# Optimization experiments

Hardware: AMD Instinct MI355X
Metric: run time of the kernel (lower is better)

The kernel has to match this reference:

```python
import jax, jax.numpy as jnp
import numpy as np

NEG_INF = -9.0e15  # matches torch's -9000000000000000.0 mask value
ALPHA = 0.2        # LeakyReLU negative slope from init_kwargs


def setup_inputs() -> dict:
    key = jax.random.key(0)
    k1, k2, k3, k4, k5 = jax.random.split(key, 5)
    B, N, D, A = 64, 128, 128, 1000
    hidden = jax.random.normal(k1, (B, N, D), dtype=jnp.float32)
    adj = jax.random.randint(k2, (B, N, N), 0, 5)  # edge types 0..4 (0 = masked)
    a = jax.random.normal(k3, (D, 4), dtype=jnp.float32) * 0.1  # stacked a_0..a_3
    A_attr_sess = jax.random.uniform(k4, (B, N, A), dtype=jnp.float32)
    attr_embedding = jax.random.normal(k5, (A, D), dtype=jnp.float32)
    return {"hidden": hidden, "adj": adj, "a": a,
            "A_attr_sess": A_attr_sess, "attr_embedding": attr_embedding}


def reference(hidden, adj, a, A_attr_sess, attr_embedding):
    # a_input[b,i,j,:] = leaky_relu(h[b,i,:] * h[b,j,:])  -> [B,N,N,D]
    a_input = jax.nn.leaky_relu(hidden[:, :, None, :] * hidden[:, None, :, :],
                                negative_slope=ALPHA)
    # four edge-type scores in one contraction: [B,N,N,4]
    e = jnp.einsum('bijd,dk->bijk', a_input, a)
    # masked selection by adjacency edge type (later writes override earlier)
    alpha = jnp.full(adj.shape, NEG_INF, dtype=e.dtype)
    alpha = jnp.where(adj == 1, e[..., 0], alpha)
    alpha = jnp.where(adj == 2, e[..., 1], alpha)
    alpha = jnp.where(adj == 3, e[..., 2], alpha)
    alpha = jnp.where(adj == 4, e[..., 3], alpha)
    attn = jax.nn.softmax(alpha, axis=-1)        # [B,N,N]
    output = jnp.einsum('bij,bjd->bid', attn, hidden)  # [B,N,D]
    attr_sess = jnp.einsum('bna,ad->bnd', A_attr_sess, attr_embedding)
    return output, attr_sess
```

## Files before the change

### kernel.cpp

```cpp
#include <hip/hip_runtime.h>

#define BB 64
#define NN 128
#define DD 128
#define AA 1000
#define KPAD 1024
#define NEG_INF (-9.0e15f)

typedef __attribute__((ext_vector_type(8))) short short8;
typedef __attribute__((ext_vector_type(4))) float floatx4;
typedef __attribute__((ext_vector_type(4))) unsigned int uintx4;
typedef __attribute__((ext_vector_type(2))) unsigned int uintx2;

__device__ __forceinline__ float bflo(unsigned int u) { return __uint_as_float(u << 16); }
__device__ __forceinline__ float bfhi(unsigned int u) { return __uint_as_float(u & 0xffff0000u); }
__device__ __forceinline__ unsigned int packbf(float f0, float f1) {
  return (__float_as_uint(f0) >> 16) | (__float_as_uint(f1) & 0xffff0000u);
}
__device__ __forceinline__ unsigned short bf_rne(float f) {
  unsigned int u = __float_as_uint(f);
  return (unsigned short)((u + 0x7fffu + ((u >> 16) & 1u)) >> 16);
}
__device__ __forceinline__ unsigned int packbf_rne(float f0, float f1) {
  return (unsigned int)bf_rne(f0) | ((unsigned int)bf_rne(f1) << 16);
}
__device__ __forceinline__ short8 u2s(uintx4 v) {
  union { uintx4 u; short8 s; } x; x.u = v; return x.s;
}

__global__ __launch_bounds__(256) void prep_kernel(
    const float* __restrict__ hidden, const float* __restrict__ emb,
    unsigned short* __restrict__ ET, unsigned short* __restrict__ HTg)
{
  __shared__ float hsf[NN * 129];
  const int t = threadIdx.x;
  const int bid = blockIdx.x;
  if (bid < BB) {
    const float* hb = hidden + (size_t)bid * NN * DD;
    #pragma unroll
    for (int u = 0; u < 16; ++u) {
      int e = u * 1024 + t * 4;
      float4 v = *reinterpret_cast<const float4*>(hb + e);
      int r = e >> 7, c = e & 127;
      float* d = &hsf[r * 129 + c];
      d[0] = v.x; d[1] = v.y; d[2] = v.z; d[3] = v.w;
    }
    __syncthreads();
    unsigned short* ht16 = HTg + (size_t)bid * NN * DD;
    #pragma unroll
    for (int u = 0; u < 8; ++u) {
      int e = u * 2048 + t * 8;
      int dI = e >> 7, il = e & 127;
      float x[8];
      #pragma unroll
      for (int j = 0; j < 8; ++j) x[j] = hsf[(il + j) * 129 + dI];
      uintx4 o;
      o.x = packbf_rne(x[0], x[1]); o.y = packbf_rne(x[2], x[3]);
      o.z = packbf_rne(x[4], x[5]); o.w = packbf_rne(x[6], x[7]);
      *reinterpret_cast<uintx4*>(ht16 + e) = o;
    }
  } else {
    const int k0 = (bid - BB) * 32;
    #pragma unroll
    for (int u = 0; u < 4; ++u) {
      int e = u * 1024 + t * 4;
      int r = e >> 7, c = e & 127;
      float4 z = {0.f, 0.f, 0.f, 0.f};
      float4 v = (k0 + r < AA)
          ? *reinterpret_cast<const float4*>(emb + (size_t)(k0 + r) * DD + c) : z;
      float* d = &hsf[r * 129 + c];
      d[0] = v.x; d[1] = v.y; d[2] = v.z; d[3] = v.w;
    }
    __syncthreads();
    int c = t >> 1, j0 = (t & 1) * 16;
    float x[16];
    #pragma unroll
    for (int j = 0; j < 16; ++j) x[j] = hsf[(j0 + j) * 129 + c];
    uintx4 o0, o1;
    o0.x = packbf_rne(x[0], x[1]);  o0.y = packbf_rne(x[2], x[3]);
    o0.z = packbf_rne(x[4], x[5]);  o0.w = packbf_rne(x[6], x[7]);
    o1.x = packbf_rne(x[8], x[9]);  o1.y = packbf_rne(x[10], x[11]);
    o1.z = packbf_rne(x[12], x[13]); o1.w = packbf_rne(x[14], x[15]);
    unsigned short* dst = ET + (size_t)c * KPAD + k0 + j0;
    *reinterpret_cast<uintx4*>(dst) = o0;
    *reinterpret_cast<uintx4*>(dst + 8) = o1;
  }
}

struct AttnSmem {
  __align__(16) unsigned short Hs[NN * 128];
  union {
    __align__(16) unsigned short As[4 * 16 * 256];
    struct {
      __align__(16) float Sa[16 * 129];
      __align__(16) unsigned short W[16 * 128];
    } sw;
  } u2;
  __align__(16) float saf[4 * 256];
};

#define BK 64
struct AttrSmem {
  __align__(16) unsigned short ETs[2][DD * BK];
  __align__(16) unsigned short As2[2][16 * BK];
};

union FusedSmem { AttnSmem a; AttrSmem g; };

__device__ __forceinline__ void attn_body(
    AttnSmem& s, const float* __restrict__ hidden,
    const int* __restrict__ adj, const float* __restrict__ amat,
    const unsigned short* __restrict__ HTg, float* __restrict__ out0,
    int wid)
{
  const int t = threadIdx.x;
  const int L = t & 63, w = t >> 6;
  const int lr = L & 15, lq = L >> 4;
  const int b = wid >> 3;
  const int i0 = (wid & 7) * 16;

  const int* adjb = adj + ((size_t)b * NN + i0) * NN;
  int adjv[8];
  #pragma unroll
  for (int nt = 0; nt < 2; ++nt)
    #pragma unroll
    for (int r = 0; r < 4; ++r)
      adjv[nt * 4 + r] = adjb[(lq * 4 + r) * NN + w * 32 + nt * 16 + lr];

  const float* hb = hidden + (size_t)b * NN * DD;
  #pragma unroll
  for (int u = 0; u < 8; ++u) {
    int id = u * 256 + t;
    int r = id >> 4, c = id & 15;
    const float* src = hb + r * 128 + c * 8;
    float4 v0 = *reinterpret_cast<const float4*>(src);
    float4 v1 = *reinterpret_cast<const float4*>(src + 4);
    uintx4 o;
    o.x = packbf_rne(v0.x, v0.y); o.y = packbf_rne(v0.z, v0.w);
    o.z = packbf_rne(v1.x, v1.y); o.w = packbf_rne(v1.z, v1.w);
    *reinterpret_cast<uintx4*>(&s.Hs[r * 128 + ((c ^ (r & 15)) << 3)]) = o;
  }
  {
    float v1 = amat[t], v2 = amat[t + 256];
    int dI = t >> 2, k = t & 3;
    s.saf[k * 256 + dI] = 0.6f * v1;
    s.saf[k * 256 + 128 + dI] = 0.4f * v1;
    s.saf[k * 256 + 64 + dI] = 0.6f * v2;
    s.saf[k * 256 + 192 + dI] = 0.4f * v2;
  }
  __syncthreads();

  #pragma unroll
  for (int u = 0; u < 8; ++u) {
    int id = u * 256 + t;
    int k = id >> 9, ii = (id >> 5) & 15, c = id & 31;
    int srow = i0 + ii;
    int dchunk = c & 15;
    uintx4 hv = *reinterpret_cast<const uintx4*>(
        &s.Hs[srow * 128 + ((dchunk ^ (srow & 15)) << 3)]);
    if (c & 16) {
      hv.x &= 0x7fff7fffu; hv.y &= 0x7fff7fffu;
      hv.z &= 0x7fff7fffu; hv.w &= 0x7fff7fffu;
    }
    const float* sf = &s.saf[k * 256 + c * 8];
    uintx4 o;
    o.x = packbf(bflo(hv.x) * sf[0], bfhi(hv.x) * sf[1]);
    o.y = packbf(bflo(hv.y) * sf[2], bfhi(hv.y) * sf[3]);
    o.z = packbf(bflo(hv.z) * sf[4], bfhi(hv.z) * sf[5]);
    o.w = packbf(bflo(hv.w) * sf[6], bfhi(hv.w) * sf[7]);
    *reinterpret_cast<uintx4*>(&s.u2.As[k * 4096 + ii * 256 + ((c ^ ii) << 3)]) = o;
  }
  __syncthreads();

  floatx4 acc[4][2];
  #pragma unroll
  for (int k = 0; k < 4; ++k)
    #pragma unroll
    for (int nt = 0; nt < 2; ++nt) acc[k][nt] = floatx4{0.f, 0.f, 0.f, 0.f};

  #pragma unroll
  for (int kt = 0; kt < 8; ++kt) {
    int ca = lq + 4 * kt;
    short8 afr[4];
    #pragma unroll
    for (int k = 0; k < 4; ++k)
      afr[k] = *reinterpret_cast<const short8*>(
          &s.u2.As[k * 4096 + lr * 256 + ((ca ^ lr) << 3)]);
    int cb = lq + 4 * (kt & 3);
    short8 bfr[2];
    #pragma unroll
    for (int nt = 0; nt < 2; ++nt) {
      int jrow = w * 32 + nt * 16 + lr;
      uintx4 hv = *reinterpret_cast<const uintx4*>(
          &s.Hs[jrow * 128 + ((cb ^ (jrow & 15)) << 3)]);
      if (kt >= 4) {
        hv.x &= 0x7fff7fffu; hv.y &= 0x7fff7fffu;
        hv.z &= 0x7fff7fffu; hv.w &= 0x7fff7fffu;
      }
      bfr[nt] = u2s(hv);
    }
    #pragma unroll
    for (int k = 0; k < 4; ++k)
      #pragma unroll
      for (int nt = 0; nt < 2; ++nt)
        acc[k][nt] = __builtin_amdgcn_mfma_f32_16x16x32_bf16(
            afr[k], bfr[nt], acc[k][nt], 0, 0, 0);
  }
  __syncthreads();

  short8 pvb[2][4];
  const unsigned short* ht = HTg + (size_t)b * NN * DD;
  #pragma unroll
  for (int nt = 0; nt < 2; ++nt)
    #pragma unroll
    for (int kt = 0; kt < 4; ++kt) {
      int dI = w * 32 + nt * 16 + lr;
      pvb[nt][kt] = *reinterpret_cast<const short8*>(ht + dI * 128 + kt * 32 + lq * 8);
    }

  #pragma unroll
  for (int nt = 0; nt < 2; ++nt)
    #pragma unroll
    for (int r = 0; r < 4; ++r) {
      int ii = lq * 4 + r;
      int j = w * 32 + nt * 16 + lr;
      int ad = adjv[nt * 4 + r];
      float al = NEG_INF;
      al = (ad == 1) ? acc[0][nt][r] : al;
      al = (ad == 2) ? acc[1][nt][r] : al;
      al = (ad == 3) ? acc[2][nt][r] : al;
      al = (ad == 4) ? acc[3][nt][r] : al;
      s.u2.sw.Sa[ii * 129 + j] = al;
    }
  __syncthreads();

  #pragma unroll
  for (int p = 0; p < 4; ++p) {
    int ii = w * 4 + p;
    float a1 = s.u2.sw.Sa[ii * 129 + L];
    float a2 = s.u2.sw.Sa[ii * 129 + 64 + L];
    float m = fmaxf(a1, a2);
    #pragma unroll
    for (int off = 32; off > 0; off >>= 1) m = fmaxf(m, __shfl_xor(m, off, 64));
    float e1 = __expf(fmaxf(a1 - m, -80.f));
    float e2 = __expf(fmaxf(a2 - m, -80.f));
    float ss = e1 + e2;
    #pragma unroll
    for (int off = 32; off > 0; off >>= 1) ss += __shfl_xor(ss, off, 64);
    float inv = 1.f / ss;
    int j2 = L + 64;
    s.u2.sw.W[ii * 128 + (((L >> 3) ^ ii) << 3) + (L & 7)] = bf_rne(e1 * inv);
    s.u2.sw.W[ii * 128 + (((j2 >> 3) ^ ii) << 3) + (j2 & 7)] = bf_rne(e2 * inv);
  }
  __syncthreads();

  floatx4 oacc[2];
  oacc[0] = floatx4{0.f, 0.f, 0.f, 0.f};
  oacc[1] = floatx4{0.f, 0.f, 0.f, 0.f};
  #pragma unroll
  for (int kt = 0; kt < 4; ++kt) {
    int c = lq + 4 * kt;
    short8 wf = *reinterpret_cast<const short8*>(
        &s.u2.sw.W[lr * 128 + ((c ^ lr) << 3)]);
    #pragma unroll
    for (int nt = 0; nt < 2; ++nt)
      oacc[nt] = __builtin_amdgcn_mfma_f32_16x16x32_bf16(
          wf, pvb[nt][kt], oacc[nt], 0, 0, 0);
  }
  float* ob = out0 + ((size_t)b * NN + i0) * DD;
  #pragma unroll
  for (int nt = 0; nt < 2; ++nt)
    #pragma unroll
    for (int r = 0; r < 4; ++r)
      ob[(lq * 4 + r) * DD + w * 32 + nt * 16 + lr] = oacc[nt][r];
}

__device__ __forceinline__ void attr_body(
    AttrSmem& s, const float* __restrict__ Aattr,
    const unsigned short* __restrict__ ET, float* __restrict__ out1,
    int wid)
{
  const int t = threadIdx.x;
  const int L = t & 63, w = t >> 6;
  const int lr = L & 15, lq = L >> 4;
  const int r0 = wid * 16;

  const int ar = t >> 4;
  const int ak = (t & 15) * 4;
  const int ec = t >> 1, ej0 = (t & 1) * 4;
  const float* arow = Aattr + (size_t)(r0 + ar) * AA;
  const unsigned short* erow = ET + (size_t)ec * KPAD;

  float4 paA, paB;
  uintx4 peA[4], peB[4];

#define ATTR_FETCH(PA, PE, IT) do {                                          \
    int kb = (IT) * BK; int k4 = kb + ak;                                    \
    float4 z = {0.f, 0.f, 0.f, 0.f};                                        \
    PA = (k4 < AA) ? *reinterpret_cast<const float4*>(arow + k4) : z;        \
    _Pragma("unroll")                                                        \
    for (int q = 0; q < 4; ++q)                                              \
      PE[q] = *reinterpret_cast<const uintx4*>(erow + kb + (ej0 + q) * 8);   \
  } while (0)

#define ATTR_STAGE(PA, PE, BUF) do {                                         \
    uintx2 o; o.x = packbf(PA.x, PA.y); o.y = packbf(PA.z, PA.w);            \
    int cidx = ak >> 3, half = ak & 7;                                       \
    *reinterpret_cast<uintx2*>(                                              \
        &s.As2[BUF][ar * BK + ((cidx ^ (ar & 7)) << 3) + half]) = o;         \
    _Pragma("unroll")                                                        \
    for (int q = 0; q < 4; ++q)                                              \
      *reinterpret_cast<uintx4*>(                                            \
          &s.ETs[BUF][ec * BK + (((ej0 + q) ^ (ec & 7)) << 3)]) = PE[q];     \
  } while (0)

#define ATTR_COMPUTE(BUF) do {                                               \
    _Pragma("unroll")                                                        \
    for (int ks = 0; ks < 2; ++ks) {                                         \
      int c = lq + 4 * ks;                                                   \
      short8 af = *reinterpret_cast<const short8*>(                          \
          &s.As2[BUF][lr * BK + ((c ^ (lr & 7)) << 3)]);                     \
      _Pragma("unroll")                                                      \
      for (int nt = 0; nt < 2; ++nt) {                                       \
        int n = w * 32 + nt * 16 + lr;                                       \
        short8 bf = *reinterpret_cast<const short8*>(                        \
            &s.ETs[BUF][n * BK + ((c ^ (n & 7)) << 3)]);                     \
        acc[nt] = __builtin_amdgcn_mfma_f32_16x16x32_bf16(                   \
            af, bf, acc[nt], 0, 0, 0);                                       \
      }                                                                      \
    }                                                                        \
  } while (0)

  floatx4 acc[2];
  acc[0] = floatx4{0.f, 0.f, 0.f, 0.f};
  acc[1] = floatx4{0.f, 0.f, 0.f, 0.f};

  ATTR_FETCH(paA, peA, 0);
  ATTR_FETCH(paB, peB, 1);
  for (int ith = 0; ith < 8; ++ith) {
    ATTR_STAGE(paA, peA, 0);
    __syncthreads();
    if (ith < 7) ATTR_FETCH(paA, peA, 2 * ith + 2);
    ATTR_COMPUTE(0);
    ATTR_STAGE(paB, peB, 1);
    __syncthreads();
    if (ith < 7) ATTR_FETCH(paB, peB, 2 * ith + 3);
    ATTR_COMPUTE(1);
  }
#undef ATTR_FETCH
#undef ATTR_STAGE
#undef ATTR_COMPUTE

  float* ob = out1 + (size_t)r0 * DD;
  #pragma unroll
  for (int nt = 0; nt < 2; ++nt)
    #pragma unroll
    for (int r = 0; r < 4; ++r)
      ob[(lq * 4 + r) * DD + w * 32 + nt * 16 + lr] = acc[nt][r];
}

__global__ __launch_bounds__(256, 2) void fused_kernel(
    const float* __restrict__ hidden, const int* __restrict__ adj,
    const float* __restrict__ amat, const float* __restrict__ Aattr,
    const unsigned short* __restrict__ ET, const unsigned short* __restrict__ HTg,
    float* __restrict__ out0, float* __restrict__ out1)
{
  __shared__ FusedSmem sm;
  const int bid = blockIdx.x;
  const int wid = (bid & 7) * 64 + (bid >> 3);
  if (wid & 1) {
    attn_body(sm.a, hidden, adj, amat, HTg, out0, wid);
    __syncthreads();
    attr_body(sm.g, Aattr, ET, out1, wid);
  } else {
    attr_body(sm.g, Aattr, ET, out1, wid);
    __syncthreads();
    attn_body(sm.a, hidden, adj, amat, HTg, out0, wid);
  }
}

extern "C" void kernel_launch(void* const* d_in, const int* in_sizes, int n_in,
                              void* d_out, int out_size, void* d_ws, size_t ws_size,
                              hipStream_t stream) {
  const float* hidden = (const float*)d_in[0];
  const int*   adj    = (const int*)d_in[1];
  const float* amat   = (const float*)d_in[2];
  const float* Aattr  = (const float*)d_in[3];
  const float* emb    = (const float*)d_in[4];

  float* out0 = (float*)d_out;
  float* out1 = out0 + (size_t)BB * NN * DD;

  unsigned short* ET  = (unsigned short*)d_ws;
  unsigned short* HTg = ET + (size_t)DD * KPAD;

  prep_kernel<<<BB + 32, 256, 0, stream>>>(hidden, emb, ET, HTg);
  fused_kernel<<<512, 256, 0, stream>>>(hidden, adj, amat, Aattr, ET, HTg,
                                        out0, out1);
}
```

Before: 104.4 us.

## Precompute bf16 operands in prep kernel and split attn/attr into separate blocks

The prep kernel now also writes bf16 hidden and the pre-scaled LeakyReLU A-operand (four edge types) to global workspace. The fused kernel can then load MFMA fragments straight from global memory instead of staging them through LDS. The attention and attribute GEMMs now run in separate blocks, 1024 in total with occupancy 4, instead of being serialized inside one block. The attribute GEMM drops its LDS double buffering in favour of register prefetch. This cuts LDS use and syncs and raises occupancy, at the cost of extra workspace traffic and more prep work.

```diff
diff --git a/kernel.cpp b/kernel.cpp
--- a/kernel.cpp
+++ b/kernel.cpp
@@ -10,7 +10,6 @@
 typedef __attribute__((ext_vector_type(8))) short short8;
 typedef __attribute__((ext_vector_type(4))) float floatx4;
 typedef __attribute__((ext_vector_type(4))) unsigned int uintx4;
-typedef __attribute__((ext_vector_type(2))) unsigned int uintx2;
 
 __device__ __forceinline__ float bflo(unsigned int u) { return __uint_as_float(u << 16); }
 __device__ __forceinline__ float bfhi(unsigned int u) { return __uint_as_float(u & 0xffff0000u); }
@@ -27,12 +26,18 @@
 __device__ __forceinline__ short8 u2s(uintx4 v) {
   union { uintx4 u; short8 s; } x; x.u = v; return x.s;
 }
+__device__ __forceinline__ float rne_f(float x, unsigned int msk) {
+  return __uint_as_float(((unsigned int)bf_rne(x) & msk) << 16);
+}
 
 __global__ __launch_bounds__(256) void prep_kernel(
     const float* __restrict__ hidden, const float* __restrict__ emb,
-    unsigned short* __restrict__ ET, unsigned short* __restrict__ HTg)
+    const float* __restrict__ amat,
+    unsigned short* __restrict__ ET, unsigned short* __restrict__ HTg,
+    unsigned short* __restrict__ Hg, unsigned short* __restrict__ Asg)
 {
   __shared__ float hsf[NN * 129];
+  __shared__ float safk[256];
   const int t = threadIdx.x;
   const int bid = blockIdx.x;
   if (bid < BB) {
@@ -59,7 +64,18 @@
       o.z = packbf_rne(x[4], x[5]); o.w = packbf_rne(x[6], x[7]);
       *reinterpret_cast<uintx4*>(ht16 + e) = o;
     }
-  } else {
+    unsigned short* hg = Hg + (size_t)bid * NN * DD;
+    #pragma unroll
+    for (int u = 0; u < 8; ++u) {
+      int id = u * 256 + t;
+      int r = id >> 4, c = id & 15;
+      const float* src = &hsf[r * 129 + c * 8];
+      uintx4 o;
+      o.x = packbf_rne(src[0], src[1]); o.y = packbf_rne(src[2], src[3]);
+      o.z = packbf_rne(src[4], src[5]); o.w = packbf_rne(src[6], src[7]);
+      *reinterpret_cast<uintx4*>(hg + r * 128 + c * 8) = o;
+    }
+  } else if (bid < BB + 32) {
     const int k0 = (bid - BB) * 32;
     #pragma unroll
     for (int u = 0; u < 4; ++u) {
@@ -84,298 +100,229 @@
     unsigned short* dst = ET + (size_t)c * KPAD + k0 + j0;
     *reinterpret_cast<uintx4*>(dst) = o0;
     *reinterpret_cast<uintx4*>(dst + 8) = o1;
+  } else {
+    const int idx = bid - BB - 32;
+    const int b = idx >> 2, k = idx & 3;
+    safk[t] = ((t & 128) ? 0.4f : 0.6f) * amat[(t & 127) * 4 + k];
+    __syncthreads();
+    const float* hb = hidden + (size_t)b * NN * DD;
+    unsigned short* ag = Asg + ((size_t)b * NN * 4 + k) * 256;
+    #pragma unroll
+    for (int u = 0; u < 16; ++u) {
+      int id = u * 256 + t;
+      int i = id >> 5, c = id & 31;
+      const float* src = hb + i * DD + (c & 15) * 8;
+      float4 v0 = *reinterpret_cast<const float4*>(src);
+      float4 v1 = *reinterpret_cast<const float4*>(src + 4);
+      unsigned int msk = (c & 16) ? 0x7fffu : 0xffffu;
+      float ve0 = rne_f(v0.x, msk), ve1 = rne_f(v0.y, msk);
+      float ve2 = rne_f(v0.z, msk), ve3 = rne_f(v0.w, msk);
+      float ve4 = rne_f(v1.x, msk), ve5 = rne_f(v1.y, msk);
+      float ve6 = rne_f(v1.z, msk), ve7 = rne_f(v1.w, msk);
+      const float* sf = &safk[c * 8];
+      uintx4 o;
+      o.x = packbf(ve0 * sf[0], ve1 * sf[1]);
+      o.y = packbf(ve2 * sf[2], ve3 * sf[3]);
+      o.z = packbf(ve4 * sf[4], ve5 * sf[5]);
+      o.w = packbf(ve6 * sf[6], ve7 * sf[7]);
+      *reinterpret_cast<uintx4*>(ag + (size_t)i * 1024 + c * 8) = o;
+    }
   }
 }
 
-struct AttnSmem {
-  __align__(16) unsigned short Hs[NN * 128];
-  union {
-    __align__(16) unsigned short As[4 * 16 * 256];
-    struct {
-      __align__(16) float Sa[16 * 129];
-      __align__(16) unsigned short W[16 * 128];
-    } sw;
-  } u2;
-  __align__(16) float saf[4 * 256];
+struct FS {
+  __align__(16) float Sa[16 * 129];
+  __align__(16) unsigned short W[16 * 128];
 };
 
-#define BK 64
-struct AttrSmem {
-  __align__(16) unsigned short ETs[2][DD * BK];
-  __align__(16) unsigned short As2[2][16 * BK];
-};
-
-union FusedSmem { AttnSmem a; AttrSmem g; };
-
-__device__ __forceinline__ void attn_body(
-    AttnSmem& s, const float* __restrict__ hidden,
-    const int* __restrict__ adj, const float* __restrict__ amat,
-    const unsigned short* __restrict__ HTg, float* __restrict__ out0,
-    int wid)
+__global__ __launch_bounds__(256, 4) void fused_kernel(
+    const int* __restrict__ adj, const float* __restrict__ Aattr,
+    const unsigned short* __restrict__ ET, const unsigned short* __restrict__ HTg,
+    const unsigned short* __restrict__ Hg, const unsigned short* __restrict__ Asg,
+    float* __restrict__ out0, float* __restrict__ out1)
 {
+  __shared__ FS s;
   const int t = threadIdx.x;
   const int L = t & 63, w = t >> 6;
   const int lr = L & 15, lq = L >> 4;
-  const int b = wid >> 3;
-  const int i0 = (wid & 7) * 16;
-
-  const int* adjb = adj + ((size_t)b * NN + i0) * NN;
-  int adjv[8];
-  #pragma unroll
-  for (int nt = 0; nt < 2; ++nt)
-    #pragma unroll
-    for (int r = 0; r < 4; ++r)
-      adjv[nt * 4 + r] = adjb[(lq * 4 + r) * NN + w * 32 + nt * 16 + lr];
-
-  const float* hb = hidden + (size_t)b * NN * DD;
-  #pragma unroll
-  for (int u = 0; u < 8; ++u) {
-    int id = u * 256 + t;
-    int r = id >> 4, c = id & 15;
-    const float* src = hb + r * 128 + c * 8;
-    float4 v0 = *reinterpret_cast<const float4*>(src);
-    float4 v1 = *reinterpret_cast<const float4*>(src + 4);
-    uintx4 o;
-    o.x = packbf_rne(v0.x, v0.y); o.y = packbf_rne(v0.z, v0.w);
-    o.z = packbf_rne(v1.x, v1.y); o.w = packbf_rne(v1.z, v1.w);
-    *reinterpret_cast<uintx4*>(&s.Hs[r * 128 + ((c ^ (r & 15)) << 3)]) = o;
-  }
-  {
-    float v1 = amat[t], v2 = amat[t + 256];
-    int dI = t >> 2, k = t & 3;
-    s.saf[k * 256 + dI] = 0.6f * v1;
-    s.saf[k * 256 + 128 + dI] = 0.4f * v1;
-    s.saf[k * 256 + 64 + dI] = 0.6f * v2;
-    s.saf[k * 256 + 192 + dI] = 0.4f * v2;
-  }
-  __syncthreads();
-
-  #pragma unroll
-  for (int u = 0; u < 8; ++u) {
-    int id = u * 256 + t;
-    int k = id >> 9, ii = (id >> 5) & 15, c = id & 31;
-    int srow = i0 + ii;
-    int dchunk = c & 15;
-    uintx4 hv = *reinterpret_cast<const uintx4*>(
-        &s.Hs[srow * 128 + ((dchunk ^ (srow & 15)) << 3)]);
-    if (c & 16) {
-      hv.x &= 0x7fff7fffu; hv.y &= 0x7fff7fffu;
-      hv.z &= 0x7fff7fffu; hv.w &= 0x7fff7fffu;
-    }
-    const float* sf = &s.saf[k * 256 + c * 8];
-    uintx4 o;
-    o.x = packbf(bflo(hv.x) * sf[0], bfhi(hv.x) * sf[1]);
-    o.y = packbf(bflo(hv.y) * sf[2], bfhi(hv.y) * sf[3]);
-    o.z = packbf(bflo(hv.z) * sf[4], bfhi(hv.z) * sf[5]);
-    o.w = packbf(bflo(hv.w) * sf[6], bfhi(hv.w) * sf[7]);
-    *reinterpret_cast<uintx4*>(&s.u2.As[k * 4096 + ii * 256 + ((c ^ ii) << 3)]) = o;
-  }
-  __syncthreads();
-
-  floatx4 acc[4][2];
-  #pragma unroll
-  for (int k = 0; k < 4; ++k)
-    #pragma unroll
-    for (int nt = 0; nt < 2; ++nt) acc[k][nt] = floatx4{0.f, 0.f, 0.f, 0.f};
-
-  #pragma unroll
-  for (int kt = 0; kt < 8; ++kt) {
-    int ca = lq + 4 * kt;
-    short8 afr[4];
+  const int bid = blockIdx.x;
+  const int wid = (bid & 7) * 128 + (bid >> 3);
+  const int tile = wid >> 1;
+
+  if ((wid & 1) == 0) {
+    const int b = tile >> 3;
+    const int i0 = (tile & 7) * 16;
+
+    const int* adjb = adj + ((size_t)b * NN + i0) * NN;
+    int adjv[8];
+    #pragma unroll
+    for (int nt = 0; nt < 2; ++nt)
+      #pragma unroll
+      for (int r = 0; r < 4; ++r)
+        adjv[nt * 4 + r] = adjb[(lq * 4 + r) * NN + w * 32 + nt * 16 + lr];
+
+    const unsigned short* hg = Hg + (size_t)b * NN * DD;
+    uintx4 hvq[2][4];
+    #pragma unroll
+    for (int nt = 0; nt < 2; ++nt)
+      #pragma unroll
+      for (int q = 0; q < 4; ++q) {
+        int jrow = w * 32 + nt * 16 + lr;
+        hvq[nt][q] = *reinterpret_cast<const uintx4*>(
+            hg + jrow * 128 + (lq + 4 * q) * 8);
+      }
+
+    const unsigned short* ag = Asg + ((size_t)(b * NN + i0 + lr)) * 4 * 256;
+    floatx4 acc[4][2];
     #pragma unroll
     for (int k = 0; k < 4; ++k)
-      afr[k] = *reinterpret_cast<const short8*>(
-          &s.u2.As[k * 4096 + lr * 256 + ((ca ^ lr) << 3)]);
-    int cb = lq + 4 * (kt & 3);
-    short8 bfr[2];
-    #pragma unroll
-    for (int nt = 0; nt < 2; ++nt) {
-      int jrow = w * 32 + nt * 16 + lr;
-      uintx4 hv = *reinterpret_cast<const uintx4*>(
-          &s.Hs[jrow * 128 + ((cb ^ (jrow & 15)) << 3)]);
-      if (kt >= 4) {
-        hv.x &= 0x7fff7fffu; hv.y &= 0x7fff7fffu;
-        hv.z &= 0x7fff7fffu; hv.w &= 0x7fff7fffu;
+      #pragma unroll
+      for (int nt = 0; nt < 2; ++nt) acc[k][nt] = floatx4{0.f, 0.f, 0.f, 0.f};
+
+    #pragma unroll
+    for (int kt = 0; kt < 8; ++kt) {
+      int ca = lq + 4 * kt;
+      short8 afr[4];
+      #pragma unroll
+      for (int k = 0; k < 4; ++k)
+        afr[k] = *reinterpret_cast<const short8*>(ag + k * 256 + ca * 8);
+      #pragma unroll
+      for (int nt = 0; nt < 2; ++nt) {
+        uintx4 hv = hvq[nt][kt & 3];
+        if (kt >= 4) {
+          hv.x &= 0x7fff7fffu; hv.y &= 0x7fff7fffu;
+          hv.z &= 0x7fff7fffu; hv.w &= 0x7fff7fffu;
+        }
+        short8 bfr = u2s(hv);
+        #pragma unroll
+        for (int k = 0; k < 4; ++k)
+          acc[k][nt] = __builtin_amdgcn_mfma_f32_16x16x32_bf16(
+              afr[k], bfr, acc[k][nt], 0, 0, 0);
       }
-      bfr[nt] = u2s(hv);
-    }
-    #pragma unroll
-    for (int k = 0; k < 4; ++k)
-      #pragma unroll
-      for (int nt = 0; nt < 2; ++nt)
-        acc[k][nt] = __builtin_amdgcn_mfma_f32_16x16x32_bf16(
-            afr[k], bfr[nt], acc[k][nt], 0, 0, 0);
-  }
-  __syncthreads();
-
-  short8 pvb[2][4];
-  const unsigned short* ht = HTg + (size_t)b * NN * DD;
-  #pragma unroll
-  for (int nt = 0; nt < 2; ++nt)
+    }
+
+    short8 pvb[2][4];
+    const unsigned short* ht = HTg + (size_t)b * NN * DD;
+    #pragma unroll
+    for (int nt = 0; nt < 2; ++nt)
+      #pragma unroll
+      for (int kt = 0; kt < 4; ++kt) {
+        int dI = w * 32 + nt * 16 + lr;
+        pvb[nt][kt] = *reinterpret_cast<const short8*>(
+            ht + dI * 128 + kt * 32 + lq * 8);
+      }
+
+    #pragma unroll
+    for (int nt = 0; nt < 2; ++nt)
+      #pragma unroll
+      for (int r = 0; r < 4; ++r) {
+        int ii = lq * 4 + r;
+        int j = w * 32 + nt * 16 + lr;
+        int ad = adjv[nt * 4 + r];
+        float al = NEG_INF;
+        al = (ad == 1) ? acc[0][nt][r] : al;
+        al = (ad == 2) ? acc[1][nt][r] : al;
+        al = (ad == 3) ? acc[2][nt][r] : al;
+        al = (ad == 4) ? acc[3][nt][r] : al;
+        s.Sa[ii * 129 + j] = al;
+      }
+    __syncthreads();
+
+    #pragma unroll
+    for (int p = 0; p < 4; ++p) {
+      int ii = w * 4 + p;
+      float a1 = s.Sa[ii * 129 + L];
+      float a2 = s.Sa[ii * 129 + 64 + L];
+      float m = fmaxf(a1, a2);
+      #pragma unroll
+      for (int off = 32; off > 0; off >>= 1) m = fmaxf(m, __shfl_xor(m, off, 64));
+      float e1 = __expf(fmaxf(a1 - m, -80.f));
+      float e2 = __expf(fmaxf(a2 - m, -80.f));
+      float ss = e1 + e2;
+      #pragma unroll
+      for (int off = 32; off > 0; off >>= 1) ss += __shfl_xor(ss, off, 64);
+      float inv = 1.f / ss;
+      int j2 = L + 64;
+      s.W[ii * 128 + (((L >> 3) ^ ii) << 3) + (L & 7)] = bf_rne(e1 * inv);
+      s.W[ii * 128 + (((j2 >> 3) ^ ii) << 3) + (j2 & 7)] = bf_rne(e2 * inv);
+    }
+    __syncthreads();
+
+    floatx4 oacc0 = floatx4{0.f, 0.f, 0.f, 0.f};
+    floatx4 oacc1 = floatx4{0.f, 0.f, 0.f, 0.f};
     #pragma unroll
     for (int kt = 0; kt < 4; ++kt) {
-      int dI = w * 32 + nt * 16 + lr;
-      pvb[nt][kt] = *reinterpret_cast<const short8*>(ht + dI * 128 + kt * 32 + lq * 8);
-    }
-
-  #pragma unroll
-  for (int nt = 0; nt < 2; ++nt)
+      int c = lq + 4 * kt;
+      short8 wf = *reinterpret_cast<const short8*>(
+          &s.W[lr * 128 + ((c ^ lr) << 3)]);
+      oacc0 = __builtin_amdgcn_mfma_f32_16x16x32_bf16(wf, pvb[0][kt], oacc0, 0, 0, 0);
+      oacc1 = __builtin_amdgcn_mfma_f32_16x16x32_bf16(wf, pvb[1][kt], oacc1, 0, 0, 0);
+    }
+    float* ob = out0 + ((size_t)b * NN + i0) * DD;
     #pragma unroll
     for (int r = 0; r < 4; ++r) {
-      int ii = lq * 4 + r;
-      int j = w * 32 + nt * 16 + lr;
-      int ad = adjv[nt * 4 + r];
-      float al = NEG_INF;
-      al = (ad == 1) ? acc[0][nt][r] : al;
-      al = (ad == 2) ? acc[1][nt][r] : al;
-      al = (ad == 3) ? acc[2][nt][r] : al;
-      al = (ad == 4) ? acc[3][nt][r] : al;
-      s.u2.sw.Sa[ii * 129 + j] = al;
-    }
-  __syncthreads();
-
-  #pragma unroll
-  for (int p = 0; p < 4; ++p) {
-    int ii = w * 4 + p;
-    float a1 = s.u2.sw.Sa[ii * 129 + L];
-    float a2 = s.u2.sw.Sa[ii * 129 + 64 + L];
-    float m = fmaxf(a1, a2);
-    #pragma unroll
-    for (int off = 32; off > 0; off >>= 1) m = fmaxf(m, __shfl_xor(m, off, 64));
-    float e1 = __expf(fmaxf(a1 - m, -80.f));
-    float e2 = __expf(fmaxf(a2 - m, -80.f));
-    float ss = e1 + e2;
-    #pragma unroll
-    for (int off = 32; off > 0; off >>= 1) ss += __shfl_xor(ss, off, 64);
-    float inv = 1.f / ss;
-    int j2 = L + 64;
-    s.u2.sw.W[ii * 128 + (((L >> 3) ^ ii) << 3) + (L & 7)] = bf_rne(e1 * inv);
-    s.u2.sw.W[ii * 128 + (((j2 >> 3) ^ ii) << 3) + (j2 & 7)] = bf_rne(e2 * inv);
-  }
-  __syncthreads();
-
-  floatx4 oacc[2];
-  oacc[0] = floatx4{0.f, 0.f, 0.f, 0.f};
-  oacc[1] = floatx4{0.f, 0.f, 0.f, 0.f};
-  #pragma unroll
-  for (int kt = 0; kt < 4; ++kt) {
-    int c = lq + 4 * kt;
-    short8 wf = *reinterpret_cast<const short8*>(
-        &s.u2.sw.W[lr * 128 + ((c ^ lr) << 3)]);
-    #pragma unroll
-    for (int nt = 0; nt < 2; ++nt)
-      oacc[nt] = __builtin_amdgcn_mfma_f32_16x16x32_bf16(
-          wf, pvb[nt][kt], oacc[nt], 0, 0, 0);
-  }
-  float* ob = out0 + ((size_t)b * NN + i0) * DD;
-  #pragma unroll
-  for (int nt = 0; nt < 2; ++nt)
-    #pragma unroll
-    for (int r = 0; r < 4; ++r)
-      ob[(lq * 4 + r) * DD + w * 32 + nt * 16 + lr] = oacc[nt][r];
-}
-
-__device__ __forceinline__ void attr_body(
-    AttrSmem& s, const float* __restrict__ Aattr,
-    const unsigned short* __restrict__ ET, float* __restrict__ out1,
-    int wid)
-{
-  const int t = threadIdx.x;
-  const int L = t & 63, w = t >> 6;
-  const int lr = L & 15, lq = L >> 4;
-  const int r0 = wid * 16;
-
-  const int ar = t >> 4;
-  const int ak = (t & 15) * 4;
-  const int ec = t >> 1, ej0 = (t & 1) * 4;
-  const float* arow = Aattr + (size_t)(r0 + ar) * AA;
-  const unsigned short* erow = ET + (size_t)ec * KPAD;
-
-  float4 paA, paB;
-  uintx4 peA[4], peB[4];
-
-#define ATTR_FETCH(PA, PE, IT) do {                                          \
-    int kb = (IT) * BK; int k4 = kb + ak;                                    \
+      ob[(lq * 4 + r) * DD + w * 32 + lr] = oacc0[r];
+      ob[(lq * 4 + r) * DD + w * 32 + 16 + lr] = oacc1[r];
+    }
+  } else {
+    const int r0 = tile * 16;
+    const float* arow = Aattr + (size_t)(r0 + lr) * AA;
+    const unsigned short* e0 = ET + (size_t)(w * 32 + lr) * KPAD;
+    const unsigned short* e1 = ET + (size_t)(w * 32 + 16 + lr) * KPAD;
+
+    float4 paA[4], paB[4];
+    uintx4 peA[4], peB[4];
+    floatx4 acc0 = floatx4{0.f, 0.f, 0.f, 0.f};
+    floatx4 acc1 = floatx4{0.f, 0.f, 0.f, 0.f};
+
+#define AFETCH(PA, PE, IT) do {                                              \
+    int kb = (IT) * 64;                                                      \
     float4 z = {0.f, 0.f, 0.f, 0.f};                                        \
-    PA = (k4 < AA) ? *reinterpret_cast<const float4*>(arow + k4) : z;        \
-    _Pragma("unroll")                                                        \
-    for (int q = 0; q < 4; ++q)                                              \
-      PE[q] = *reinterpret_cast<const uintx4*>(erow + kb + (ej0 + q) * 8);   \
-  } while (0)
-
-#define ATTR_STAGE(PA, PE, BUF) do {                                         \
-    uintx2 o; o.x = packbf(PA.x, PA.y); o.y = packbf(PA.z, PA.w);            \
-    int cidx = ak >> 3, half = ak & 7;                                       \
-    *reinterpret_cast<uintx2*>(                                              \
-        &s.As2[BUF][ar * BK + ((cidx ^ (ar & 7)) << 3) + half]) = o;         \
-    _Pragma("unroll")                                                        \
-    for (int q = 0; q < 4; ++q)                                              \
-      *reinterpret_cast<uintx4*>(                                            \
-          &s.ETs[BUF][ec * BK + (((ej0 + q) ^ (ec & 7)) << 3)]) = PE[q];     \
-  } while (0)
-
-#define ATTR_COMPUTE(BUF) do {                                               \
     _Pragma("unroll")                                                        \
     for (int ks = 0; ks < 2; ++ks) {                                         \
-      int c = lq + 4 * ks;                                                   \
-      short8 af = *reinterpret_cast<const short8*>(                          \
-          &s.As2[BUF][lr * BK + ((c ^ (lr & 7)) << 3)]);                     \
-      _Pragma("unroll")                                                      \
-      for (int nt = 0; nt < 2; ++nt) {                                       \
-        int n = w * 32 + nt * 16 + lr;                                       \
-        short8 bf = *reinterpret_cast<const short8*>(                        \
-            &s.ETs[BUF][n * BK + ((c ^ (n & 7)) << 3)]);                     \
-        acc[nt] = __builtin_amdgcn_mfma_f32_16x16x32_bf16(                   \
-            af, bf, acc[nt], 0, 0, 0);                                       \
-      }                                                                      \
+      int k4 = kb + (lq + 4 * ks) * 8;                                       \
+      PA[ks * 2 + 0] = (k4 < AA) ? *reinterpret_cast<const float4*>(arow + k4) : z; \
+      PA[ks * 2 + 1] = (k4 + 4 < AA) ? *reinterpret_cast<const float4*>(arow + k4 + 4) : z; \
+      PE[ks * 2 + 0] = *reinterpret_cast<const uintx4*>(e0 + k4);            \
+      PE[ks * 2 + 1] = *reinterpret_cast<const uintx4*>(e1 + k4);            \
     }                                                                        \
   } while (0)
 
-  floatx4 acc[2];
-  acc[0] = floatx4{0.f, 0.f, 0.f, 0.f};
-  acc[1] = floatx4{0.f, 0.f, 0.f, 0.f};
-
-  ATTR_FETCH(paA, peA, 0);
-  ATTR_FETCH(paB, peB, 1);
-  for (int ith = 0; ith < 8; ++ith) {
-    ATTR_STAGE(paA, peA, 0);
-    __syncthreads();
-    if (ith < 7) ATTR_FETCH(paA, peA, 2 * ith + 2);
-    ATTR_COMPUTE(0);
-    ATTR_STAGE(paB, peB, 1);
-    __syncthreads();
-    if (ith < 7) ATTR_FETCH(paB, peB, 2 * ith + 3);
-    ATTR_COMPUTE(1);
-  }
-#undef ATTR_FETCH
-#undef ATTR_STAGE
-#undef ATTR_COMPUTE
-
-  float* ob = out1 + (size_t)r0 * DD;
-  #pragma unroll
-  for (int nt = 0; nt < 2; ++nt)
-    #pragma unroll
-    for (int r = 0; r < 4; ++r)
-      ob[(lq * 4 + r) * DD + w * 32 + nt * 16 + lr] = acc[nt][r];
-}
-
-__global__ __launch_bounds__(256, 2) void fused_kernel(
-    const float* __restrict__ hidden, const int* __restrict__ adj,
-    const float* __restrict__ amat, const float* __restrict__ Aattr,
-    const unsigned short* __restrict__ ET, const unsigned short* __restrict__ HTg,
-    float* __restrict__ out0, float* __restrict__ out1)
-{
-  __shared__ FusedSmem sm;
-  const int bid = blockIdx.x;
-  const int wid = (bid & 7) * 64 + (bid >> 3);
-  if (wid & 1) {
-    attn_body(sm.a, hidden, adj, amat, HTg, out0, wid);
-    __syncthreads();
-    attr_body(sm.g, Aattr, ET, out1, wid);
-  } else {
-    attr_body(sm.g, Aattr, ET, out1, wid);
-    __syncthreads();
-    attn_body(sm.a, hidden, adj, amat, HTg, out0, wid);
+#define ABODY(PA, PE, IT) do {                                               \
+    short8 af0, af1, bf00, bf01, bf10, bf11;                                 \
+    {                                                                        \
+      uintx4 a0, a1;                                                         \
+      a0.x = packbf(PA[0].x, PA[0].y); a0.y = packbf(PA[0].z, PA[0].w);      \
+      a0.z = packbf(PA[1].x, PA[1].y); a0.w = packbf(PA[1].z, PA[1].w);      \
+      a1.x = packbf(PA[2].x, PA[2].y); a1.y = packbf(PA[2].z, PA[2].w);      \
+      a1.z = packbf(PA[3].x, PA[3].y); a1.w = packbf(PA[3].z, PA[3].w);      \
+      af0 = u2s(a0); af1 = u2s(a1);                                          \
+      bf00 = u2s(PE[0]); bf01 = u2s(PE[1]);                                  \
+      bf10 = u2s(PE[2]); bf11 = u2s(PE[3]);                                  \
+    }                                                                        \
+    if ((IT) < 14) AFETCH(PA, PE, (IT) + 2);                                 \
+    acc0 = __builtin_amdgcn_mfma_f32_16x16x32_bf16(af0, bf00, acc0, 0, 0, 0); \
+    acc1 = __builtin_amdgcn_mfma_f32_16x16x32_bf16(af0, bf01, acc1, 0, 0, 0); \
+    acc0 = __builtin_amdgcn_mfma_f32_16x16x32_bf16(af1, bf10, acc0, 0, 0, 0); \
+    acc1 = __builtin_amdgcn_mfma_f32_16x16x32_bf16(af1, bf11, acc1, 0, 0, 0); \
+  } while (0)
+
+    AFETCH(paA, peA, 0);
+    AFETCH(paB, peB, 1);
+    #pragma unroll
+    for (int ith = 0; ith < 8; ++ith) {
+      ABODY(paA, peA, 2 * ith);
+      ABODY(paB, peB, 2 * ith + 1);
+    }
+#undef AFETCH
+#undef ABODY
+
+    float* ob = out1 + (size_t)r0 * DD;
+    #pragma unroll
+    for (int r = 0; r < 4; ++r) {
+      ob[(lq * 4 + r) * DD + w * 32 + lr] = acc0[r];
+      ob[(lq * 4 + r) * DD + w * 32 + 16 + lr] = acc1[r];
+    }
   }
 }
 
@@ -393,8 +340,11 @@
 
   unsigned short* ET  = (unsigned short*)d_ws;
   unsigned short* HTg = ET + (size_t)DD * KPAD;
-
-  prep_kernel<<<BB + 32, 256, 0, stream>>>(hidden, emb, ET, HTg);
-  fused_kernel<<<512, 256, 0, stream>>>(hidden, adj, amat, Aattr, ET, HTg,
-                                        out0, out1);
-}
+  unsigned short* Hg  = HTg + (size_t)BB * NN * DD;
+  unsigned short* Asg = Hg + (size_t)BB * NN * DD;
+
+  prep_kernel<<<BB + 32 + 256, 256, 0, stream>>>(hidden, emb, amat,
+                                                 ET, HTg, Hg, Asg);
+  fused_kernel<<<1024, 256, 0, stream>>>(adj, Aattr, ET, HTg, Hg, Asg,
+                                         out0, out1);
+}
```

After: 130.1 us. +24.6%, slower.
